# Kernel optimization log

Hardware: AMD Instinct MI355X
Metric: run time of the kernel (lower is better)

## Reference

```python
import jax, jax.numpy as jnp
import numpy as np

SIGMA = 0.1
GAMMA = 1.0 / (SIGMA * SIGMA)  # keops-style gauss kernel: exp(-|x-y|^2 / sigma^2)
B, N, D = 1, 8192, 3


def setup_inputs() -> dict:
    key = jax.random.key(0)
    k1, k2 = jax.random.split(key)
    control_points = jax.random.uniform(k1, (B, N, D), dtype=jnp.float32)
    mom = jax.random.normal(k2, (B, N, D), dtype=jnp.float32) * 0.1
    return {"mom": mom, "control_points": control_points}


def _pairwise_dist2(x, y):
    # x:[B,N,D], y:[B,M,D] -> [B,N,M] squared distances (no N x M x D intermediate)
    x2 = jnp.sum(x * x, -1)  # [B,N]
    y2 = jnp.sum(y * y, -1)  # [B,M]
    xy = jnp.einsum('bnd,bmd->bnm', x, y)
    return x2[:, :, None] + y2[:, None, :] - 2.0 * xy


def gauss_kernel(x, y, b):
    # K(x,y) b : [B,N,d]
    K = jnp.exp(-GAMMA * _pairwise_dist2(x, y))  # [B,N,M]
    return jnp.einsum('bnm,bmd->bnd', K, b)


def gauss_grad_kernel(p, x):
    # dH/dx_i = sum_j d/dx_i[exp(-g|x_i-x_j|^2)] <p_i,p_j>
    #         = -2g * sum_j K_ij <p_i,p_j> (x_i - x_j)
    K = jnp.exp(-GAMMA * _pairwise_dist2(x, x))        # [B,N,N]
    W = K * jnp.einsum('bnd,bmd->bnm', p, p)           # [B,N,N] weighted by <p_i,p_j>
    row_sum = jnp.sum(W, -1)                           # [B,N]
    Wx = jnp.einsum('bnm,bmd->bnd', W, x)              # [B,N,D]
    return (-2.0 * GAMMA) * (x * row_sum[:, :, None] - Wx)


def reference(mom, control_points):
    # variational_evolve: (dp/dt, dx/dt)
    dmom = -gauss_grad_kernel(mom, control_points)
    dx = gauss_kernel(control_points, control_points, mom)
    return (dmom, dx)
```

## Files before the change

kernel.cpp:

```cpp
#include <hip/hip_runtime.h>


#define TPB 256
constexpr float GAMMA_C = 100.0f;
constexpr float LOG2E_C = 1.4426950408889634f;
constexpr float SB_C    = 2.0f * GAMMA_C * LOG2E_C;
constexpr float SC_C    = -GAMMA_C * LOG2E_C;
constexpr float LN2_C   = 0.69314718055994531f;

__global__ __launch_bounds__(TPB, 8) void lddmm_partial(
    const float* __restrict__ mom, const float* __restrict__ xpt,
    float* __restrict__ ws, int N, int SEG, int JT) {
  extern __shared__ float4 smem[];
  float4* sA = smem;
  float4* sP = smem + JT;
  const int tid = threadIdx.x;
  const int seg = blockIdx.y;

  for (int t = tid; t < JT; t += TPB) {
    const int j = seg * JT + t;
    const float bx = xpt[3*j], by = xpt[3*j+1], bz = xpt[3*j+2];
    sA[t] = make_float4(SB_C*bx, SB_C*by, SB_C*bz,
                        SC_C * fmaf(bx, bx, fmaf(by, by, bz*bz)));
    sP[t] = make_float4(mom[3*j], mom[3*j+1], mom[3*j+2], 0.f);
  }
  __syncthreads();

  const int i = blockIdx.x * TPB + tid;
  const float xi  = xpt[3*i], yi  = xpt[3*i+1], zi  = xpt[3*i+2];
  const float pxi = mom[3*i], pyi = mom[3*i+1], pzi = mom[3*i+2];
  const float ci  = SC_C * fmaf(xi, xi, fmaf(yi, yi, zi*zi));

  float a = 0.f;
  float wx = 0.f, wy = 0.f, wz = 0.f;
  float gx = 0.f, gy = 0.f, gz = 0.f;

#pragma unroll 4
  for (int t = 0; t < JT; ++t) {
    const float4 A = sA[t];
    const float4 P = sP[t];
    const float arg = fmaf(A.x, xi, fmaf(A.y, yi, fmaf(A.z, zi, ci + A.w)));
    const float K   = exp2f(arg);
    const float dot = fmaf(P.x, pxi, fmaf(P.y, pyi, P.z * pzi));
    const float w   = K * dot;
    a  += w;
    wx = fmaf(w, A.x, wx); wy = fmaf(w, A.y, wy); wz = fmaf(w, A.z, wz);
    gx = fmaf(K, P.x, gx); gy = fmaf(K, P.y, gy); gz = fmaf(K, P.z, gz);
  }

  const size_t SN = (size_t)SEG * N;
  float* p = ws + (size_t)seg * N + i;
  p[0*SN] = a;
  p[1*SN] = wx; p[2*SN] = wy; p[3*SN] = wz;
  p[4*SN] = gx; p[5*SN] = gy; p[6*SN] = gz;
}

__global__ __launch_bounds__(TPB) void lddmm_reduce(
    const float* __restrict__ ws, float* __restrict__ R, int N, int SEG) {
  const int i = blockIdx.x * TPB + threadIdx.x;
  const int c = blockIdx.y;
  const float* src = ws + (size_t)c * SEG * N + i;
  float s0 = 0.f, s1 = 0.f, s2 = 0.f, s3 = 0.f;
  int s = 0;
  for (; s + 4 <= SEG; s += 4) {
    s0 += src[(size_t)(s+0)*N]; s1 += src[(size_t)(s+1)*N];
    s2 += src[(size_t)(s+2)*N]; s3 += src[(size_t)(s+3)*N];
  }
  for (; s < SEG; ++s) s0 += src[(size_t)s*N];
  R[(size_t)c * N + i] = (s0 + s1) + (s2 + s3);
}

__global__ __launch_bounds__(TPB) void lddmm_finalize(
    const float* __restrict__ R, const float* __restrict__ xpt,
    float* __restrict__ out, int N) {
  const int i = blockIdx.x * TPB + threadIdx.x;
  const float A  = R[i];
  const float WX = R[(size_t)1*N+i], WY = R[(size_t)2*N+i], WZ = R[(size_t)3*N+i];
  const float GX = R[(size_t)4*N+i], GY = R[(size_t)5*N+i], GZ = R[(size_t)6*N+i];
  const float xi = xpt[3*i], yi = xpt[3*i+1], zi = xpt[3*i+2];
  const float TGA = 2.0f * GAMMA_C * A;
  out[3*i+0] = fmaf(TGA, xi, -LN2_C * WX);
  out[3*i+1] = fmaf(TGA, yi, -LN2_C * WY);
  out[3*i+2] = fmaf(TGA, zi, -LN2_C * WZ);
  out[3*N + 3*i + 0] = GX;
  out[3*N + 3*i + 1] = GY;
  out[3*N + 3*i + 2] = GZ;
}

__global__ __launch_bounds__(TPB) void lddmm_atomic(
    const float* __restrict__ mom, const float* __restrict__ xpt,
    float* __restrict__ out, int N) {
  const int i  = blockIdx.x * TPB + threadIdx.x;
  const int jb = blockIdx.y * TPB;
  __shared__ float4 sA[TPB], sP[TPB];
  {
    const int j = jb + threadIdx.x;
    const float bx = xpt[3*j], by = xpt[3*j+1], bz = xpt[3*j+2];
    sA[threadIdx.x] = make_float4(SB_C*bx, SB_C*by, SB_C*bz,
                                  SC_C * fmaf(bx, bx, fmaf(by, by, bz*bz)));
    sP[threadIdx.x] = make_float4(mom[3*j], mom[3*j+1], mom[3*j+2], 0.f);
  }
  __syncthreads();
  const float xi = xpt[3*i], yi = xpt[3*i+1], zi = xpt[3*i+2];
  const float pxi = mom[3*i], pyi = mom[3*i+1], pzi = mom[3*i+2];
  const float ci = SC_C * fmaf(xi, xi, fmaf(yi, yi, zi*zi));
  float a=0.f, wx=0.f, wy=0.f, wz=0.f, gx=0.f, gy=0.f, gz=0.f;
#pragma unroll 4
  for (int t = 0; t < TPB; ++t) {
    const float4 A = sA[t], P = sP[t];
    const float arg = fmaf(A.x, xi, fmaf(A.y, yi, fmaf(A.z, zi, ci + A.w)));
    const float K   = exp2f(arg);
    const float dot = fmaf(P.x, pxi, fmaf(P.y, pyi, P.z * pzi));
    const float w   = K * dot;
    a += w;
    wx = fmaf(w, A.x, wx); wy = fmaf(w, A.y, wy); wz = fmaf(w, A.z, wz);
    gx = fmaf(K, P.x, gx); gy = fmaf(K, P.y, gy); gz = fmaf(K, P.z, gz);
  }
  const float TGA = 2.0f * GAMMA_C * a;
  atomicAdd(&out[3*i+0], fmaf(TGA, xi, -LN2_C * wx));
  atomicAdd(&out[3*i+1], fmaf(TGA, yi, -LN2_C * wy));
  atomicAdd(&out[3*i+2], fmaf(TGA, zi, -LN2_C * wz));
  atomicAdd(&out[3*N+3*i+0], gx);
  atomicAdd(&out[3*N+3*i+1], gy);
  atomicAdd(&out[3*N+3*i+2], gz);
}

extern "C" void kernel_launch(void* const* d_in, const int* in_sizes, int n_in,
                              void* d_out, int out_size, void* d_ws, size_t ws_size,
                              hipStream_t stream) {
  const float* mom = (const float*)d_in[0];
  const float* xpt = (const float*)d_in[1];
  float* out = (float*)d_out;
  const int N = in_sizes[0] / 3;

  auto need = [&](int s) { return (size_t)(7*s + 7) * (size_t)N * sizeof(float); };
  int SEG = 64;
  while (SEG > 2 && need(SEG) > ws_size) SEG >>= 1;

  if (need(SEG) <= ws_size) {
    const int JT = N / SEG;
    float* wsf = (float*)d_ws;
    float* R   = wsf + (size_t)7 * SEG * N;
    const size_t shmem = (size_t)JT * 2 * sizeof(float4);
    dim3 gA(N / TPB, SEG);
    lddmm_partial<<<gA, TPB, shmem, stream>>>(mom, xpt, wsf, N, SEG, JT);
    dim3 gB(N / TPB, 7);
    lddmm_reduce<<<gB, TPB, 0, stream>>>(wsf, R, N, SEG);
    lddmm_finalize<<<N / TPB, TPB, 0, stream>>>(R, xpt, out, N);
  } else {
    hipMemsetAsync(d_out, 0, (size_t)out_size * sizeof(float), stream);
    dim3 grid(N / TPB, N / TPB);
    lddmm_atomic<<<grid, TPB, 0, stream>>>(mom, xpt, out, N);
  }
}
```

Before: 107.1 us.

## Register-tile four rows per thread with packed float2 math and raw exp2

Each thread of the partial kernel now handles four i points, held as two float2 vector lanes, so every shared-memory load of a j point is reused four times. The FMAs are written with ext_vector_type(2) so they can map to packed FP32 instructions. exp2f is replaced by the raw hardware exp2 builtin in both the partial and atomic kernels, which drops the range-handling wrapper. SEG is doubled to keep the block count up now that there are fewer i blocks, at the cost of more partial data in the workspace and more work for the reduce kernel. Register pressure rises, and launch bounds drop to 4 waves per SIMD.

```diff
diff --git a/kernel.cpp b/kernel.cpp
--- a/kernel.cpp
+++ b/kernel.cpp
@@ -2,13 +2,21 @@
 
 
 #define TPB 256
+#define ITILE 4
 constexpr float GAMMA_C = 100.0f;
 constexpr float LOG2E_C = 1.4426950408889634f;
 constexpr float SB_C    = 2.0f * GAMMA_C * LOG2E_C;
 constexpr float SC_C    = -GAMMA_C * LOG2E_C;
 constexpr float LN2_C   = 0.69314718055994531f;
 
-__global__ __launch_bounds__(TPB, 8) void lddmm_partial(
+typedef float v2f __attribute__((ext_vector_type(2)));
+
+static __device__ __forceinline__ v2f splat2(float v) { return (v2f){v, v}; }
+static __device__ __forceinline__ v2f fma2(v2f a, v2f b, v2f c) {
+  return __builtin_elementwise_fma(a, b, c);
+}
+
+__global__ __launch_bounds__(TPB, 4) void lddmm_partial(
     const float* __restrict__ mom, const float* __restrict__ xpt,
     float* __restrict__ ws, int N, int SEG, int JT) {
   extern __shared__ float4 smem[];
@@ -26,33 +34,58 @@
   }
   __syncthreads();
 
-  const int i = blockIdx.x * TPB + tid;
-  const float xi  = xpt[3*i], yi  = xpt[3*i+1], zi  = xpt[3*i+2];
-  const float pxi = mom[3*i], pyi = mom[3*i+1], pzi = mom[3*i+2];
-  const float ci  = SC_C * fmaf(xi, xi, fmaf(yi, yi, zi*zi));
+  const int i0 = blockIdx.x * (TPB * ITILE) + tid;
+  const int i1 = i0 + TPB, i2 = i0 + 2*TPB, i3 = i0 + 3*TPB;
 
-  float a = 0.f;
-  float wx = 0.f, wy = 0.f, wz = 0.f;
-  float gx = 0.f, gy = 0.f, gz = 0.f;
+  const v2f xA = {xpt[3*i0],   xpt[3*i1]},   xB = {xpt[3*i2],   xpt[3*i3]};
+  const v2f yA = {xpt[3*i0+1], xpt[3*i1+1]}, yB = {xpt[3*i2+1], xpt[3*i3+1]};
+  const v2f zA = {xpt[3*i0+2], xpt[3*i1+2]}, zB = {xpt[3*i2+2], xpt[3*i3+2]};
+  const v2f pxA = {mom[3*i0],   mom[3*i1]},   pxB = {mom[3*i2],   mom[3*i3]};
+  const v2f pyA = {mom[3*i0+1], mom[3*i1+1]}, pyB = {mom[3*i2+1], mom[3*i3+1]};
+  const v2f pzA = {mom[3*i0+2], mom[3*i1+2]}, pzB = {mom[3*i2+2], mom[3*i3+2]};
+  const v2f cA = splat2(SC_C) * fma2(xA, xA, fma2(yA, yA, zA*zA));
+  const v2f cB = splat2(SC_C) * fma2(xB, xB, fma2(yB, yB, zB*zB));
+
+  v2f aA = {0,0}, wxA = {0,0}, wyA = {0,0}, wzA = {0,0};
+  v2f gxA = {0,0}, gyA = {0,0}, gzA = {0,0};
+  v2f aB = {0,0}, wxB = {0,0}, wyB = {0,0}, wzB = {0,0};
+  v2f gxB = {0,0}, gyB = {0,0}, gzB = {0,0};
 
 #pragma unroll 4
   for (int t = 0; t < JT; ++t) {
     const float4 A = sA[t];
     const float4 P = sP[t];
-    const float arg = fmaf(A.x, xi, fmaf(A.y, yi, fmaf(A.z, zi, ci + A.w)));
-    const float K   = exp2f(arg);
-    const float dot = fmaf(P.x, pxi, fmaf(P.y, pyi, P.z * pzi));
-    const float w   = K * dot;
-    a  += w;
-    wx = fmaf(w, A.x, wx); wy = fmaf(w, A.y, wy); wz = fmaf(w, A.z, wz);
-    gx = fmaf(K, P.x, gx); gy = fmaf(K, P.y, gy); gz = fmaf(K, P.z, gz);
+    const v2f Ax = splat2(A.x), Ay = splat2(A.y), Az = splat2(A.z);
+    const v2f Px = splat2(P.x), Py = splat2(P.y), Pz = splat2(P.z);
+    {
+      const v2f arg = fma2(Ax, xA, fma2(Ay, yA, fma2(Az, zA, cA + splat2(A.w))));
+      v2f K; K.x = __builtin_amdgcn_exp2f(arg.x); K.y = __builtin_amdgcn_exp2f(arg.y);
+      const v2f dot = fma2(Px, pxA, fma2(Py, pyA, Pz * pzA));
+      const v2f w = K * dot;
+      aA += w;
+      wxA = fma2(w, Ax, wxA); wyA = fma2(w, Ay, wyA); wzA = fma2(w, Az, wzA);
+      gxA = fma2(K, Px, gxA); gyA = fma2(K, Py, gyA); gzA = fma2(K, Pz, gzA);
+    }
+    {
+      const v2f arg = fma2(Ax, xB, fma2(Ay, yB, fma2(Az, zB, cB + splat2(A.w))));
+      v2f K; K.x = __builtin_amdgcn_exp2f(arg.x); K.y = __builtin_amdgcn_exp2f(arg.y);
+      const v2f dot = fma2(Px, pxB, fma2(Py, pyB, Pz * pzB));
+      const v2f w = K * dot;
+      aB += w;
+      wxB = fma2(w, Ax, wxB); wyB = fma2(w, Ay, wyB); wzB = fma2(w, Az, wzB);
+      gxB = fma2(K, Px, gxB); gyB = fma2(K, Py, gyB); gzB = fma2(K, Pz, gzB);
+    }
   }
 
   const size_t SN = (size_t)SEG * N;
-  float* p = ws + (size_t)seg * N + i;
-  p[0*SN] = a;
-  p[1*SN] = wx; p[2*SN] = wy; p[3*SN] = wz;
-  p[4*SN] = gx; p[5*SN] = gy; p[6*SN] = gz;
+  float* p = ws + (size_t)seg * N;
+  p[0*SN+i0]=aA.x;  p[0*SN+i1]=aA.y;  p[0*SN+i2]=aB.x;  p[0*SN+i3]=aB.y;
+  p[1*SN+i0]=wxA.x; p[1*SN+i1]=wxA.y; p[1*SN+i2]=wxB.x; p[1*SN+i3]=wxB.y;
+  p[2*SN+i0]=wyA.x; p[2*SN+i1]=wyA.y; p[2*SN+i2]=wyB.x; p[2*SN+i3]=wyB.y;
+  p[3*SN+i0]=wzA.x; p[3*SN+i1]=wzA.y; p[3*SN+i2]=wzB.x; p[3*SN+i3]=wzB.y;
+  p[4*SN+i0]=gxA.x; p[4*SN+i1]=gxA.y; p[4*SN+i2]=gxB.x; p[4*SN+i3]=gxB.y;
+  p[5*SN+i0]=gyA.x; p[5*SN+i1]=gyA.y; p[5*SN+i2]=gyB.x; p[5*SN+i3]=gyB.y;
+  p[6*SN+i0]=gzA.x; p[6*SN+i1]=gzA.y; p[6*SN+i2]=gzB.x; p[6*SN+i3]=gzB.y;
 }
 
 __global__ __launch_bounds__(TPB) void lddmm_reduce(
@@ -109,7 +142,7 @@
   for (int t = 0; t < TPB; ++t) {
     const float4 A = sA[t], P = sP[t];
     const float arg = fmaf(A.x, xi, fmaf(A.y, yi, fmaf(A.z, zi, ci + A.w)));
-    const float K   = exp2f(arg);
+    const float K   = __builtin_amdgcn_exp2f(arg);
     const float dot = fmaf(P.x, pxi, fmaf(P.y, pyi, P.z * pzi));
     const float w   = K * dot;
     a += w;
@@ -134,7 +167,7 @@
   const int N = in_sizes[0] / 3;
 
   auto need = [&](int s) { return (size_t)(7*s + 7) * (size_t)N * sizeof(float); };
-  int SEG = 64;
+  int SEG = 128;
   while (SEG > 2 && need(SEG) > ws_size) SEG >>= 1;
 
   if (need(SEG) <= ws_size) {
@@ -142,7 +175,7 @@
     float* wsf = (float*)d_ws;
     float* R   = wsf + (size_t)7 * SEG * N;
     const size_t shmem = (size_t)JT * 2 * sizeof(float4);
-    dim3 gA(N / TPB, SEG);
+    dim3 gA(N / (TPB * ITILE), SEG);
     lddmm_partial<<<gA, TPB, shmem, stream>>>(mom, xpt, wsf, N, SEG, JT);
     dim3 gB(N / TPB, 7);
     lddmm_reduce<<<gB, TPB, 0, stream>>>(wsf, R, N, SEG);
```

Measured after the change: 97.31 us. -9.1%, faster.

## Process two target points per thread with packed float2 FMA math

Applied to the files above, without the earlier changes.

Each thread in the partial kernel now handles two i-points, using ext_vector float2 operations so the compiler can emit packed FMA instructions. Each shared-memory source load is reused across both points. The raw hardware exp2 builtin replaces exp2f, which drops the range/denormal handling wrappers. SEG is raised to 128 so the grid keeps enough blocks after halving the x dimension, at the cost of more partial-sum traffic in the reduce step and higher register pressure (launch bounds lowered to 4 waves).

```diff
diff --git a/kernel.cpp b/kernel.cpp
--- a/kernel.cpp
+++ b/kernel.cpp
@@ -2,13 +2,21 @@
 
 
 #define TPB 256
+#define ITILE 2
 constexpr float GAMMA_C = 100.0f;
 constexpr float LOG2E_C = 1.4426950408889634f;
 constexpr float SB_C    = 2.0f * GAMMA_C * LOG2E_C;
 constexpr float SC_C    = -GAMMA_C * LOG2E_C;
 constexpr float LN2_C   = 0.69314718055994531f;
 
-__global__ __launch_bounds__(TPB, 8) void lddmm_partial(
+typedef float v2f __attribute__((ext_vector_type(2)));
+
+static __device__ __forceinline__ v2f splat2(float v) { return (v2f){v, v}; }
+static __device__ __forceinline__ v2f fma2(v2f a, v2f b, v2f c) {
+  return __builtin_elementwise_fma(a, b, c);
+}
+
+__global__ __launch_bounds__(TPB, 4) void lddmm_partial(
     const float* __restrict__ mom, const float* __restrict__ xpt,
     float* __restrict__ ws, int N, int SEG, int JT) {
   extern __shared__ float4 smem[];
@@ -26,33 +34,47 @@
   }
   __syncthreads();
 
-  const int i = blockIdx.x * TPB + tid;
-  const float xi  = xpt[3*i], yi  = xpt[3*i+1], zi  = xpt[3*i+2];
-  const float pxi = mom[3*i], pyi = mom[3*i+1], pzi = mom[3*i+2];
-  const float ci  = SC_C * fmaf(xi, xi, fmaf(yi, yi, zi*zi));
+  const int i0 = blockIdx.x * (TPB * ITILE) + tid;
+  const int i1 = i0 + TPB;
 
-  float a = 0.f;
-  float wx = 0.f, wy = 0.f, wz = 0.f;
-  float gx = 0.f, gy = 0.f, gz = 0.f;
+  const v2f xi = {xpt[3*i0],   xpt[3*i1]};
+  const v2f yi = {xpt[3*i0+1], xpt[3*i1+1]};
+  const v2f zi = {xpt[3*i0+2], xpt[3*i1+2]};
+  const v2f px = {mom[3*i0],   mom[3*i1]};
+  const v2f py = {mom[3*i0+1], mom[3*i1+1]};
+  const v2f pz = {mom[3*i0+2], mom[3*i1+2]};
+  const v2f ci = splat2(SC_C) * fma2(xi, xi, fma2(yi, yi, zi*zi));
+
+  v2f a = {0,0}, wx = {0,0}, wy = {0,0}, wz = {0,0};
+  v2f gx = {0,0}, gy = {0,0}, gz = {0,0};
 
 #pragma unroll 4
   for (int t = 0; t < JT; ++t) {
     const float4 A = sA[t];
     const float4 P = sP[t];
-    const float arg = fmaf(A.x, xi, fmaf(A.y, yi, fmaf(A.z, zi, ci + A.w)));
-    const float K   = exp2f(arg);
-    const float dot = fmaf(P.x, pxi, fmaf(P.y, pyi, P.z * pzi));
-    const float w   = K * dot;
-    a  += w;
-    wx = fmaf(w, A.x, wx); wy = fmaf(w, A.y, wy); wz = fmaf(w, A.z, wz);
-    gx = fmaf(K, P.x, gx); gy = fmaf(K, P.y, gy); gz = fmaf(K, P.z, gz);
+    const v2f Ax = splat2(A.x), Ay = splat2(A.y), Az = splat2(A.z);
+    const v2f Px = splat2(P.x), Py = splat2(P.y), Pz = splat2(P.z);
+
+    const v2f arg = fma2(Ax, xi, fma2(Ay, yi, fma2(Az, zi, ci + splat2(A.w))));
+    v2f K;
+    K.x = __builtin_amdgcn_exp2f(arg.x);
+    K.y = __builtin_amdgcn_exp2f(arg.y);
+    const v2f dot = fma2(Px, px, fma2(Py, py, Pz * pz));
+    const v2f w   = K * dot;
+    a += w;
+    wx = fma2(w, Ax, wx); wy = fma2(w, Ay, wy); wz = fma2(w, Az, wz);
+    gx = fma2(K, Px, gx); gy = fma2(K, Py, gy); gz = fma2(K, Pz, gz);
   }
 
   const size_t SN = (size_t)SEG * N;
-  float* p = ws + (size_t)seg * N + i;
-  p[0*SN] = a;
-  p[1*SN] = wx; p[2*SN] = wy; p[3*SN] = wz;
-  p[4*SN] = gx; p[5*SN] = gy; p[6*SN] = gz;
+  float* p = ws + (size_t)seg * N;
+  p[0*SN+i0]=a.x;  p[0*SN+i1]=a.y;
+  p[1*SN+i0]=wx.x; p[1*SN+i1]=wx.y;
+  p[2*SN+i0]=wy.x; p[2*SN+i1]=wy.y;
+  p[3*SN+i0]=wz.x; p[3*SN+i1]=wz.y;
+  p[4*SN+i0]=gx.x; p[4*SN+i1]=gx.y;
+  p[5*SN+i0]=gy.x; p[5*SN+i1]=gy.y;
+  p[6*SN+i0]=gz.x; p[6*SN+i1]=gz.y;
 }
 
 __global__ __launch_bounds__(TPB) void lddmm_reduce(
@@ -109,7 +131,7 @@
   for (int t = 0; t < TPB; ++t) {
     const float4 A = sA[t], P = sP[t];
     const float arg = fmaf(A.x, xi, fmaf(A.y, yi, fmaf(A.z, zi, ci + A.w)));
-    const float K   = exp2f(arg);
+    const float K   = __builtin_amdgcn_exp2f(arg);
     const float dot = fmaf(P.x, pxi, fmaf(P.y, pyi, P.z * pzi));
     const float w   = K * dot;
     a += w;
@@ -134,7 +156,7 @@
   const int N = in_sizes[0] / 3;
 
   auto need = [&](int s) { return (size_t)(7*s + 7) * (size_t)N * sizeof(float); };
-  int SEG = 64;
+  int SEG = 128;
   while (SEG > 2 && need(SEG) > ws_size) SEG >>= 1;
 
   if (need(SEG) <= ws_size) {
@@ -142,7 +164,7 @@
     float* wsf = (float*)d_ws;
     float* R   = wsf + (size_t)7 * SEG * N;
     const size_t shmem = (size_t)JT * 2 * sizeof(float4);
-    dim3 gA(N / TPB, SEG);
+    dim3 gA(N / (TPB * ITILE), SEG);
     lddmm_partial<<<gA, TPB, shmem, stream>>>(mom, xpt, wsf, N, SEG, JT);
     dim3 gB(N / TPB, 7);
     lddmm_reduce<<<gB, TPB, 0, stream>>>(wsf, R, N, SEG);
```

Measured after the change: 97.96 us. -8.5%, faster.
